# Kernel tuning notes

Hardware: AMD Instinct MI355X
Metric: run time of the kernel (lower is better)

Reference implementation:

```python
import jax, jax.numpy as jnp
import numpy as np
from jax import lax

B, TZ, TT = 16, 2048, 512
D, DFF, L, V, HEADS = 256, 1024, 6, 512, 4
CH, HID, K, FLOWS, G = 256, 256, 5, 4, 256
PAD_ID = 0
NEG = -1e9
SCALE = 0.02


def setup_inputs():
    key = jax.random.key(0)
    ks = jax.random.split(key, 20)
    n = lambda i, shape, s=SCALE: jax.random.normal(ks[i], shape, jnp.float32) * s
    return {
        'z': jax.random.normal(ks[0], (B, TZ, CH), jnp.float32),
        'text': jax.random.randint(ks[1], (B, TT), 1, V),  # low=1 so no pad tokens
        'cond': jax.random.normal(ks[2], (B, G), jnp.float32),
        'embed': n(3, (V, D), 1.0),
        'wq': n(4, (L, D, D)), 'wk': n(5, (L, D, D)), 'wv': n(6, (L, D, D)), 'wo': n(7, (L, D, D)),
        'bq': jnp.zeros((L, D)), 'bk': jnp.zeros((L, D)), 'bv': jnp.zeros((L, D)), 'bo': jnp.zeros((L, D)),
        'ln1_g': jnp.ones((L, D)), 'ln1_b': jnp.zeros((L, D)),
        'ln2_g': jnp.ones((L, D)), 'ln2_b': jnp.zeros((L, D)),
        'w1': n(8, (L, D, DFF)), 'b1': jnp.zeros((L, DFF)),
        'w2': n(9, (L, DFF, D)), 'b2': jnp.zeros((L, D)),
        'mu_w': n(10, (D, D)), 'mu_b': jnp.zeros((D,)),
        'lv_w': n(11, (D, D)), 'lv_b': jnp.zeros((D,)),
        'flow_in': n(12, (FLOWS, CH // 2, HID)), 'flow_in_b': jnp.zeros((FLOWS, HID)),
        'flow_cond': n(13, (FLOWS, G, HID)),
        'flow_conv': n(14, (FLOWS, K, HID, HID)), 'flow_conv_b': jnp.zeros((FLOWS, HID)),
        'flow_out': n(15, (FLOWS, HID, CH // 2)), 'flow_out_b': jnp.zeros((FLOWS, CH // 2)),
    }


def _pos_encoding(length, d):
    pos = np.arange(length)[:, None].astype(np.float32)
    i = np.arange(d)[None, :]
    angle = pos / np.power(10000.0, (2 * (i // 2)) / d)
    pe = np.where(i % 2 == 0, np.sin(angle), np.cos(angle))
    return jnp.asarray(pe, jnp.float32)


def _ln(x, g, b):
    m = jnp.mean(x, -1, keepdims=True)
    v = jnp.var(x, -1, keepdims=True)
    return g * (x - m) * lax.rsqrt(v + 1e-6) + b


def _mha(x, wq, wk, wv, wo, bq, bk, bv, bo, bias):
    Bq, T, _ = x.shape
    dh = D // HEADS
    heads = lambda y: y.reshape(Bq, T, HEADS, dh).transpose(0, 2, 1, 3)
    q, k, v = heads(x @ wq + bq), heads(x @ wk + bk), heads(x @ wv + bv)
    scores = jnp.einsum('bhqd,bhkd->bhqk', q, k) / jnp.sqrt(jnp.float32(dh)) + bias
    attn = jax.nn.softmax(scores, axis=-1)
    out = jnp.einsum('bhqk,bhkd->bhqd', attn, v).transpose(0, 2, 1, 3).reshape(Bq, T, D)
    return out @ wo + bo


def _mas_path(logp, text_mask):
    # Viterbi monotonic alignment: each latent frame t maps to text index j(t),
    # j nondecreasing with steps in {0, 1}, start at 0, end at last valid token.
    Bq, Tz, Tt = logp.shape
    Q0 = jnp.where(jnp.arange(Tt) == 0, logp[:, 0, :], NEG)

    def fwd(Q, lt):
        Qs = jnp.concatenate([jnp.full((Bq, 1), NEG, Q.dtype), Q[:, :-1]], axis=1)
        return lt + jnp.maximum(Q, Qs), Qs > Q  # choice True => came from j-1

    _, choices = lax.scan(fwd, Q0, jnp.swapaxes(logp, 0, 1)[1:])  # [Tz-1,B,Tt]
    j_last = jnp.sum(text_mask, axis=1).astype(jnp.int32) - 1

    def bwd(j, ch):
        c = jnp.take_along_axis(ch, j[:, None], axis=1)[:, 0]
        jp = j - c.astype(jnp.int32)
        return jp, jp

    _, path_rev = lax.scan(bwd, j_last, choices[::-1])
    path = jnp.concatenate([path_rev[::-1], j_last[None]], axis=0)  # [Tz,B]
    return jnp.swapaxes(path, 0, 1)


def _forward(z, text, cond, embed, wq, wk, wv, wo, bq, bk, bv, bo, ln1_g, ln1_b, ln2_g, ln2_b,
             w1, b1, w2, b2, mu_w, mu_b, lv_w, lv_b,
             flow_in, flow_in_b, flow_cond, flow_conv, flow_conv_b, flow_out, flow_out_b):
    text_mask = text != PAD_ID  # [B,TT]
    bias = jnp.where(text_mask[:, None, None, :], 0.0, NEG)
    # text encoder: scaled embedding + sinusoidal PE + post-LN transformer blocks
    h = embed[text] * jnp.sqrt(jnp.float32(D)) + _pos_encoding(TT, D)[None]
    for l in range(L):
        h = _ln(h + _mha(h, wq[l], wk[l], wv[l], wo[l], bq[l], bk[l], bv[l], bo[l], bias), ln1_g[l], ln1_b[l])
        ffn = jax.nn.relu(h @ w1[l] + b1[l]) @ w2[l] + b2[l]
        h = _ln(h + ffn, ln2_g[l], ln2_b[l])
    mu = h @ mu_w + mu_b
    logvar = h @ lv_w + lv_b
    # residual coupling flows (mean-only, conditioned on global vector)
    zc = z
    for f in range(FLOWS):
        x0, x1 = jnp.split(zc, 2, axis=-1)
        hh = x0 @ flow_in[f] + flow_in_b[f] + (cond @ flow_cond[f])[:, None, :]
        hh = jnp.tanh(lax.conv_general_dilated(hh, flow_conv[f], (1,), 'SAME', rhs_dilation=(1,),
                                               dimension_numbers=('NWC', 'WIO', 'NWC')) + flow_conv_b[f])
        m = hh @ flow_out[f] + flow_out_b[f]
        zc = jnp.concatenate([x1 + m, x0], axis=-1)  # coupling + flip
    # gaussian log-likelihood between latent frames and text distributions
    spr = jnp.exp(-logvar)  # [B,TT,D]
    nc1 = jnp.sum(-0.5 * jnp.log(2.0 * jnp.pi) - 0.5 * logvar, axis=-1)  # [B,TT]
    nc2 = jnp.einsum('btd,bjd->btj', -0.5 * zc * zc, spr)
    nc3 = jnp.einsum('btd,bjd->btj', zc, mu * spr)
    nc4 = jnp.sum(-0.5 * mu * mu * spr, axis=-1)  # [B,TT]
    logp = nc1[:, None, :] + nc2 + nc3 + nc4[:, None, :]  # [B,TZ,TT]
    logp = jnp.where(text_mask[:, None, :], logp, NEG)
    path = _mas_path(logp, text_mask)  # [B,TZ] int32
    ctx = mu[jnp.arange(B)[:, None], path]  # expand text mu along latent time
    return ctx, h


def reference(z, text, cond, embed, wq, wk, wv, wo, bq, bk, bv, bo, ln1_g, ln1_b, ln2_g, ln2_b,
              w1, b1, w2, b2, mu_w, mu_b, lv_w, lv_b,
              flow_in, flow_in_b, flow_cond, flow_conv, flow_conv_b, flow_out, flow_out_b):
    return _forward(z, text, cond, embed, wq, wk, wv, wo, bq, bk, bv, bo, ln1_g, ln1_b, ln2_g, ln2_b,
                    w1, b1, w2, b2, mu_w, mu_b, lv_w, lv_b,
                    flow_in, flow_in_b, flow_cond, flow_conv, flow_conv_b, flow_out, flow_out_b)
```

## Files before the change

### kernel.cpp

```cpp
#include <hip/hip_runtime.h>

#define BB 16
#define TZ_ 2048
#define TT_ 512
#define D_ 256
#define DFF_ 1024
#define L_ 6
#define HEADS_ 4
#define DH_ 64
#define CH_ 256
#define HID_ 256
#define KCV 5
#define FLOWS_ 4
#define G_ 256
#define NEGF (-1000000000.0f)
#define LOG2PI 1.8378770664093453f

typedef unsigned short u16;
typedef __attribute__((ext_vector_type(8))) short short8v;
typedef __attribute__((ext_vector_type(4))) float f32x4;

__device__ __forceinline__ float wsum(float v){
#pragma unroll
  for (int o = 32; o; o >>= 1) v += __shfl_xor(v, o);
  return v;
}
__device__ __forceinline__ u16 f2bf(float x){
  unsigned u = __float_as_uint(x);
  return (u16)((u + 0x7FFFu + ((u >> 16) & 1u)) >> 16);
}
__device__ __forceinline__ float bf2f(u16 h){
  return __uint_as_float(((unsigned)h) << 16);
}
__device__ __forceinline__ unsigned pk2f(float a, float b){
  return __builtin_amdgcn_perm(__float_as_uint(b), __float_as_uint(a), 0x07060302u);
}
__device__ __forceinline__ float trnc(float f){
  return __uint_as_float(__float_as_uint(f) & 0xFFFF0000u);
}
__device__ __forceinline__ void cvt8t(float4 x, float4 y, uint4 &hi, uint4 &lo){
  hi.x = pk2f(x.x, x.y); hi.y = pk2f(x.z, x.w);
  hi.z = pk2f(y.x, y.y); hi.w = pk2f(y.z, y.w);
  float r0 = x.x - trnc(x.x), r1 = x.y - trnc(x.y), r2 = x.z - trnc(x.z), r3 = x.w - trnc(x.w);
  float r4 = y.x - trnc(y.x), r5 = y.y - trnc(y.y), r6 = y.z - trnc(y.z), r7 = y.w - trnc(y.w);
  lo.x = pk2f(r0, r1); lo.y = pk2f(r2, r3); lo.z = pk2f(r4, r5); lo.w = pk2f(r6, r7);
}
__device__ __forceinline__ unsigned rneh(float f){
  unsigned v = __float_as_uint(f);
  return (v + 0x7FFFu + ((v >> 16) & 1u)) & 0xFFFF0000u;
}
__device__ __forceinline__ void cvt8r(float4 x, float4 y, uint4 &hi, uint4 &lo){
  unsigned h0=rneh(x.x), h1=rneh(x.y), h2=rneh(x.z), h3=rneh(x.w);
  unsigned h4=rneh(y.x), h5=rneh(y.y), h6=rneh(y.z), h7=rneh(y.w);
  hi.x = h1 | (h0>>16); hi.y = h3 | (h2>>16); hi.z = h5 | (h4>>16); hi.w = h7 | (h6>>16);
  float r0 = x.x - __uint_as_float(h0), r1 = x.y - __uint_as_float(h1);
  float r2 = x.z - __uint_as_float(h2), r3 = x.w - __uint_as_float(h3);
  float r4 = y.x - __uint_as_float(h4), r5 = y.y - __uint_as_float(h5);
  float r6 = y.z - __uint_as_float(h6), r7 = y.w - __uint_as_float(h7);
  lo.x = pk2f(r0, r1); lo.y = pk2f(r2, r3); lo.z = pk2f(r4, r5); lo.w = pk2f(r6, r7);
}

__global__ void k_pe(float* __restrict__ pe){
  int t = blockIdx.x, d = threadIdx.x;
  double e = (double)(2*(d>>1)) / (double)D_;
  double ang = (double)t * pow(10000.0, -e);
  pe[t*D_ + d] = (float)(((d&1)==0) ? sin(ang) : cos(ang));
}
__global__ void k_embed(const int* __restrict__ text, const float* __restrict__ emb,
                        const float* __restrict__ pe, float* __restrict__ h){
  int row = blockIdx.x, d = threadIdx.x;
  h[(size_t)row*D_ + d] = emb[(size_t)text[row]*D_ + d]*16.0f + pe[(row%TT_)*D_ + d];
}

__global__ __launch_bounds__(256) void k_wt(
  const float* __restrict__ wq, const float* __restrict__ wk,
  const float* __restrict__ wv, const float* __restrict__ wo,
  const float* __restrict__ mu_w, const float* __restrict__ lv_w,
  const float* __restrict__ w1, const float* __restrict__ w2,
  float* __restrict__ QKVT, float* __restrict__ OT, float* __restrict__ MULVT,
  float* __restrict__ W1T, float* __restrict__ W2T)
{
  __shared__ float td[64][65];
  const int s = blockIdx.y, tile = blockIdx.x, t = threadIdx.x;
  const float* inb; float* outb; int istride, ostride;
  if (s < 24){
    int l = s>>2, wsel = s&3;
    const float* w = (wsel==0?wq:wsel==1?wk:wsel==2?wv:wo);
    inb = w + (size_t)l*65536; istride = 256;
    if (wsel < 3) outb = QKVT + (size_t)l*196608 + wsel*65536;
    else          outb = OT   + (size_t)l*65536;
    ostride = 256;
  } else if (s < 26){
    inb = (s==24 ? mu_w : lv_w); istride = 256;
    outb = MULVT + (size_t)(s-24)*65536; ostride = 256;
  } else if (s < 50){
    int idx = s-26, l = idx>>2, b2 = idx&3;
    inb = w1 + (size_t)l*262144 + b2*256; istride = 1024;
    outb = W1T + (size_t)l*262144 + (size_t)b2*65536; ostride = 256;
  } else {
    int idx = s-50, l = idx>>2, b2 = idx&3;
    inb = w2 + (size_t)l*262144 + (size_t)b2*65536; istride = 256;
    outb = W2T + (size_t)l*262144 + b2*256; ostride = 1024;
  }
  const int kt = (tile>>2)*64, nt = (tile&3)*64;
  const int r = t>>2, cq = (t&3)*16;
#pragma unroll
  for (int c=0;c<16;c+=4){
    float4 v = *(const float4*)(inb + (size_t)(kt + r)*istride + nt + cq + c);
    td[r][cq+c+0]=v.x; td[r][cq+c+1]=v.y; td[r][cq+c+2]=v.z; td[r][cq+c+3]=v.w;
  }
  __syncthreads();
#pragma unroll
  for (int c=0;c<16;c+=4){
    float4 v = make_float4(td[cq+c+0][r], td[cq+c+1][r], td[cq+c+2][r], td[cq+c+3][r]);
    *(float4*)(outb + (size_t)(nt + r)*ostride + kt + cq + c) = v;
  }
}

__global__ __launch_bounds__(256) void k_vt(const float* __restrict__ QKV, float* __restrict__ VT){
  __shared__ float td[64][65];
  const int b = blockIdx.z, dt = blockIdx.x, jt = blockIdx.y, t = threadIdx.x;
  const float* inb = QKV + (size_t)b*512*768 + 512;
  float* outb = VT + (size_t)b*131072;
  const int r = t>>2, cq = (t&3)*16;
#pragma unroll
  for (int c=0;c<16;c+=4){
    float4 v = *(const float4*)(inb + (size_t)(jt*64 + r)*768 + dt*64 + cq + c);
    td[r][cq+c+0]=v.x; td[r][cq+c+1]=v.y; td[r][cq+c+2]=v.z; td[r][cq+c+3]=v.w;
  }
  __syncthreads();
#pragma unroll
  for (int c=0;c<16;c+=4){
    float4 v = make_float4(td[cq+c+0][r], td[cq+c+1][r], td[cq+c+2][r], td[cq+c+3][r]);
    *(float4*)(outb + (size_t)(dt*64 + r)*512 + jt*64 + cq + c) = v;
  }
}

__global__ void k_bcat(const float* __restrict__ bq, const float* __restrict__ bk,
                       const float* __restrict__ bv, const float* __restrict__ mu_b,
                       const float* __restrict__ lv_b,
                       float* __restrict__ BQKV, float* __restrict__ MULVB){
  int i = blockIdx.x*256 + threadIdx.x;
  if (i < 4608){
    int l = i/768, c = i%768;
    float v = c<256 ? bq[l*256+c] : (c<512 ? bk[l*256+c-256] : bv[l*256+c-512]);
    BQKV[i] = v;
  } else if (i < 5120){
    int c = i-4608;
    MULVB[c] = c<256 ? mu_b[c] : lv_b[c-256];
  }
}

template<int WN, int EPI, int AM, int BMD>
__global__ __launch_bounds__(256,2) void k_mg(
  const void* __restrict__ Ap, const void* __restrict__ ApL, int lda, int azhi, int azlo,
  const void* __restrict__ Bp, const void* __restrict__ BpL, int ldb, int bzhi, int bzlo,
  const float* __restrict__ bias, const int* __restrict__ text,
  const float* __restrict__ nc1v, const float* __restrict__ nc4v,
  float* __restrict__ C, int ldc, int czhi, int czlo, int K)
{
  constexpr int BN = WN*32;
  __shared__ u16 AH[4096], AL[4096];
  __shared__ u16 BH[BN*32], BL[BN*32];
  char* AHB=(char*)AH; char* ALB=(char*)AL; char* BHB=(char*)BH; char* BLB=(char*)BL;
  const int t = threadIdx.x, z = blockIdx.z;
  const int m0 = blockIdx.y*128, n0 = blockIdx.x*BN;
  const size_t aoff = (size_t)(z>>2)*azhi + (size_t)(z&3)*azlo;
  const size_t boff = (size_t)(z>>2)*bzhi + (size_t)(z&3)*bzlo;
  const size_t coff = (size_t)(z>>2)*czhi + (size_t)(z&3)*czlo;
  const int w = t>>6, l = t&63;
  const int wr = (w>>1)*64, wc = (w&1)*(WN*16);
  const int lr = l&15, lg = l>>4;
  const int srow = t>>1, sseg = t&1;
  const int q  = (srow>>1)&3;
  const int wo0 = srow*64 + ((((sseg<<1)|0)^q)<<4);
  const int wo1 = srow*64 + ((((sseg<<1)|1)^q)<<4);
  const bool bact = (WN==4) || (t < 128);
  const int qa = ((wr+lr)>>1)&3, qb2 = ((wc+lr)>>1)&3;
  const int raBase = (wr+lr)*64 + ((lg^qa)<<4);
  const int rbBase = (wc+lr)*64 + ((lg^qb2)<<4);

  const float* Af = nullptr; const u16* AfH = nullptr; const u16* AfL = nullptr;
  if constexpr (AM==0 || AM==2){ Af = (const float*)Ap + aoff; }
  else { AfH = (const u16*)Ap + aoff; AfL = (const u16*)ApL + aoff; }
  const float* Bf = nullptr; const u16* BfH = nullptr; const u16* BfL = nullptr;
  if constexpr (BMD==0){ Bf = (const float*)Bp + boff; }
  else { BfH = (const u16*)Bp + boff; BfL = (const u16*)BpL + boff; }

  float4 sa0, sa1, sa2, sa3;
  uint4  pah0, pah1, pal0, pal1;
  float4 sb0, sb1, sb2, sb3;
  uint4  pbh0, pbh1, pbl0, pbl1;

  auto LOADA = [&](int kk){
    if constexpr (AM==0){
      const float* p = Af + (size_t)(m0+srow)*lda + kk + sseg*16;
      sa0=*(const float4*)p; sa1=*(const float4*)(p+4);
      sa2=*(const float4*)(p+8); sa3=*(const float4*)(p+12);
    } else if constexpr (AM==1){
      const u16* ph = AfH + (size_t)(m0+srow)*lda + kk + sseg*16;
      const u16* pl = AfL + (size_t)(m0+srow)*lda + kk + sseg*16;
      pah0 = *(const uint4*)ph; pah1 = *(const uint4*)(ph+8);
      pal0 = *(const uint4*)pl; pal1 = *(const uint4*)(pl+8);
    } else {
      int kg = kk + sseg*16;
      const float* p = Af + (size_t)(m0+srow)*lda + (kg < 256 ? kg : kg - 256);
      sa0=*(const float4*)p; sa1=*(const float4*)(p+4);
      sa2=*(const float4*)(p+8); sa3=*(const float4*)(p+12);
    }
  };
  auto LOADB = [&](int kk){
    if constexpr (BMD==0){
      const float* p = Bf + (size_t)(n0+srow)*ldb + kk + sseg*16;
      sb0=*(const float4*)p; sb1=*(const float4*)(p+4);
      sb2=*(const float4*)(p+8); sb3=*(const float4*)(p+12);
    } else {
      const u16* ph = BfH + (size_t)(n0+srow)*ldb + kk + sseg*16;
      const u16* pl = BfL + (size_t)(n0+srow)*ldb + kk + sseg*16;
      pbh0 = *(const uint4*)ph; pbh1 = *(const uint4*)(ph+8);
      pbl0 = *(const uint4*)pl; pbl1 = *(const uint4*)(pl+8);
    }
  };
  auto WRITEA = [&](int kk){
    uint4 ahi0, ahi1, alo0, alo1;
    if constexpr (AM==0){
      cvt8t(sa0,sa1,ahi0,alo0); cvt8t(sa2,sa3,ahi1,alo1);
    } else if constexpr (AM==1){
      ahi0=pah0; ahi1=pah1; alo0=pal0; alo1=pal1;
    } else {
      float4 a0=sa0, a1=sa1, a2=sa2, a3=sa3;
      int kg = kk + sseg*16;
      if (kg >= 256){
        a0.x=-0.5f*a0.x*a0.x; a0.y=-0.5f*a0.y*a0.y; a0.z=-0.5f*a0.z*a0.z; a0.w=-0.5f*a0.w*a0.w;
        a1.x=-0.5f*a1.x*a1.x; a1.y=-0.5f*a1.y*a1.y; a1.z=-0.5f*a1.z*a1.z; a1.w=-0.5f*a1.w*a1.w;
        a2.x=-0.5f*a2.x*a2.x; a2.y=-0.5f*a2.y*a2.y; a2.z=-0.5f*a2.z*a2.z; a2.w=-0.5f*a2.w*a2.w;
        a3.x=-0.5f*a3.x*a3.x; a3.y=-0.5f*a3.y*a3.y; a3.z=-0.5f*a3.z*a3.z; a3.w=-0.5f*a3.w*a3.w;
      }
      cvt8r(a0,a1,ahi0,alo0); cvt8r(a2,a3,ahi1,alo1);
    }
    *(uint4*)(AHB + wo0) = ahi0;  *(uint4*)(AHB + wo1) = ahi1;
    *(uint4*)(ALB + wo0) = alo0;  *(uint4*)(ALB + wo1) = alo1;
  };
  auto WRITEB = [&](){
    uint4 bhi0, bhi1, blo0, blo1;
    if constexpr (BMD==0){
      cvt8t(sb0,sb1,bhi0,blo0); cvt8t(sb2,sb3,bhi1,blo1);
    } else {
      bhi0=pbh0; bhi1=pbh1; blo0=pbl0; blo1=pbl1;
    }
    *(uint4*)(BHB + wo0) = bhi0;  *(uint4*)(BHB + wo1) = bhi1;
    *(uint4*)(BLB + wo0) = blo0;  *(uint4*)(BLB + wo1) = blo1;
  };

  f32x4 acc[4][WN];
#pragma unroll
  for (int i=0;i<4;i++)
#pragma unroll
    for (int j=0;j<WN;j++) acc[i][j] = (f32x4){0.f,0.f,0.f,0.f};

  LOADA(0);
  if (bact) LOADB(0);
  for (int k0 = 0; k0 < K; k0 += 32){
    __syncthreads();
    WRITEA(k0);
    if (bact) WRITEB();
    if (k0 + 32 < K){ LOADA(k0+32); if (bact) LOADB(k0+32); }
    __syncthreads();
    short8v fah[4], fal[4], fbh[WN], fbl[WN];
#pragma unroll
    for (int i=0;i<4;i++){
      fah[i] = *(short8v*)(AHB + raBase + i*1024);
      fal[i] = *(short8v*)(ALB + raBase + i*1024);
    }
#pragma unroll
    for (int j=0;j<WN;j++){
      fbh[j] = *(short8v*)(BHB + rbBase + j*1024);
      fbl[j] = *(short8v*)(BLB + rbBase + j*1024);
    }
#pragma unroll
    for (int i=0;i<4;i++)
#pragma unroll
      for (int j=0;j<WN;j++){
        acc[i][j] = __builtin_amdgcn_mfma_f32_16x16x32_bf16(fah[i], fbh[j], acc[i][j], 0,0,0);
        acc[i][j] = __builtin_amdgcn_mfma_f32_16x16x32_bf16(fal[i], fbh[j], acc[i][j], 0,0,0);
        acc[i][j] = __builtin_amdgcn_mfma_f32_16x16x32_bf16(fah[i], fbl[j], acc[i][j], 0,0,0);
      }
  }

#pragma unroll
  for (int i=0;i<4;i++){
    int mm0 = m0 + wr + i*16 + (lg<<2);
#pragma unroll
    for (int j=0;j<WN;j++){
      int nn = n0 + wc + j*16 + lr;
      float bs = 0.f; float ncb = 0.f; bool msk = true;
      if (EPI==0 || EPI==1) bs = bias ? bias[nn] : 0.f;
      if (EPI==2) msk = (text[(z>>2)*TT_ + nn] != 0);
      if (EPI==3){ ncb = nc1v[z*TT_+nn] + nc4v[z*TT_+nn]; msk = (text[z*TT_+nn] != 0); }
      f32x4 v = acc[i][j];
#pragma unroll
      for (int r=0;r<4;r++){
        int m = mm0 + r;
        float x;
        if (EPI==0)      x = v[r] + bs;
        else if (EPI==1) x = fmaxf(v[r] + bs, 0.f);
        else if (EPI==2) x = v[r]*0.125f + (msk ? 0.f : NEGF);
        else             x = msk ? (v[r] + ncb) : NEGF;
        C[coff + (size_t)m*ldc + nn] = x;
      }
    }
  }
}

__global__ __launch_bounds__(256) void k_softmax(float* __restrict__ S){
  size_t row = (size_t)blockIdx.x*4 + (threadIdx.x >> 6);
  float* p = S + row*TT_;
  int ln = threadIdx.x & 63;
  float4 a = *(float4*)(p + ln*8);
  float4 b = *(float4*)(p + ln*8 + 4);
  float x[8] = {a.x,a.y,a.z,a.w,b.x,b.y,b.z,b.w};
  float m = x[0];
#pragma unroll
  for (int i=1;i<8;i++) m = fmaxf(m, x[i]);
#pragma unroll
  for (int o2=32;o2;o2>>=1) m = fmaxf(m, __shfl_xor(m, o2));
  float s = 0.f;
#pragma unroll
  for (int i=0;i<8;i++){ x[i] = expf(x[i]-m); s += x[i]; }
  s = wsum(s);
  float inv = 1.0f/s;
  *(float4*)(p + ln*8)     = make_float4(x[0]*inv, x[1]*inv, x[2]*inv, x[3]*inv);
  *(float4*)(p + ln*8 + 4) = make_float4(x[4]*inv, x[5]*inv, x[6]*inv, x[7]*inv);
}

__global__ __launch_bounds__(256) void k_lnres(const float* __restrict__ y,
  const float* __restrict__ g, const float* __restrict__ bb, float* __restrict__ h){
  size_t row = blockIdx.x; int d = threadIdx.x;
  float v = h[row*D_ + d] + y[row*D_ + d];
  float s = wsum(v), s2 = wsum(v*v);
  __shared__ float r1[4], r2[4];
  int w = d >> 6;
  if ((d & 63) == 0){ r1[w] = s; r2[w] = s2; }
  __syncthreads();
  s  = r1[0]+r1[1]+r1[2]+r1[3];
  s2 = r2[0]+r2[1]+r2[2]+r2[3];
  float mean = s * (1.0f/D_);
  float var  = s2 * (1.0f/D_) - mean*mean;
  float inv  = rsqrtf(var + 1e-6f);
  h[row*D_ + d] = g[d]*(v - mean)*inv + bb[d];
}

__global__ __launch_bounds__(256) void k_prep(const float* __restrict__ mulv,
  u16* __restrict__ b2h, u16* __restrict__ b2l,
  float* __restrict__ nc1, float* __restrict__ nc4){
  size_t row = blockIdx.x; int d = threadIdx.x;
  float m = mulv[row*512 + d];
  float lv = mulv[row*512 + 256 + d];
  float sp = expf(-lv);
  float ms = m*sp;
  float s1 = wsum(lv), s2 = wsum(m*ms);
  __shared__ float r1[4], r2[4];
  int w = d >> 6;
  if ((d&63)==0){ r1[w]=s1; r2[w]=s2; }
  __syncthreads();
  if (d == 0){
    nc1[row] = -0.5f*((float)D_*LOG2PI + (r1[0]+r1[1]+r1[2]+r1[3]));
    nc4[row] = -0.5f*(r2[0]+r2[1]+r2[2]+r2[3]);
  }
  unsigned hm = rneh(ms);
  b2h[row*512 + d] = (u16)(hm>>16);
  b2l[row*512 + d] = f2bf(ms - __uint_as_float(hm));
  unsigned hs = rneh(sp);
  b2h[row*512 + 256 + d] = (u16)(hs>>16);
  b2l[row*512 + 256 + d] = f2bf(sp - __uint_as_float(hs));
}

__global__ __launch_bounds__(256) void k_fprep(
  const float* __restrict__ win, const float* __restrict__ wconv, const float* __restrict__ wout,
  u16* __restrict__ WITH, u16* __restrict__ WITL,
  u16* __restrict__ WCTH, u16* __restrict__ WCTL,
  u16* __restrict__ WOTH, u16* __restrict__ WOTL,
  const float* __restrict__ zsrc, u16* __restrict__ xh, u16* __restrict__ xl,
  const float* __restrict__ cond, const float* __restrict__ fcw, float* __restrict__ condp)
{
  const int bid = blockIdx.x, t = threadIdx.x;
  if (bid < 1536){
    int i = bid*256 + t;
    float wv2; u16 *dh, *dl; int idx;
    if (i < 32768){
      int n = i >> 7, k = i & 127;
      wv2 = win[k*256 + n]; dh = WITH; dl = WITL; idx = i;
    } else if (i < 360448){
      int jj = i - 32768;
      int o = jj / 1280, r = jj - o*1280;
      wv2 = wconv[(size_t)r*256 + o]; dh = WCTH; dl = WCTL; idx = jj;
    } else {
      int jj = i - 360448;
      int o = jj >> 8, k = jj & 255;
      wv2 = wout[k*128 + o]; dh = WOTH; dl = WOTL; idx = jj;
    }
    u16 hh = f2bf(wv2);
    dh[idx] = hh;
    dl[idx] = f2bf(wv2 - bf2f(hh));
  } else if (bid < 3584){
    size_t i = ((size_t)(bid-1536)*256 + t) << 3;
    size_t m2 = i >> 7; int k = (int)(i & 127);
    const float* src = zsrc + m2*256 + k;
    float4 a = *(const float4*)src; float4 b2 = *(const float4*)(src+4);
    float vv[8] = {a.x,a.y,a.z,a.w,b2.x,b2.y,b2.z,b2.w};
    short8v oh, ol;
#pragma unroll
    for (int r=0;r<8;r++){
      u16 hh = f2bf(vv[r]);
      oh[r] = (short)hh;
      ol[r] = (short)f2bf(vv[r] - bf2f(hh));
    }
    *(short8v*)(xh + i) = oh;
    *(short8v*)(xl + i) = ol;
  } else {
    int b = bid - 3584, n = t;
    float s = 0.f;
    for (int k2=0;k2<G_;k2++) s = fmaf(cond[b*G_ + k2], fcw[k2*HID_ + n], s);
    condp[b*HID_ + n] = s;
  }
}

__global__ void k_padzero2(u16* __restrict__ XpH, u16* __restrict__ XpL){
  int i = blockIdx.x*256 + threadIdx.x;
  u16* P = (i >> 14) ? XpL : XpH;
  int ii = i & 16383;
  int b = ii >> 10, rr = (ii >> 8) & 3, c = ii & 255;
  int row = (rr < 2) ? rr : (2048 + rr);
  P[((size_t)b*2052 + row)*256 + c] = 0;
}

template<int EPI, int SPLITOUT>
__global__ __launch_bounds__(256,2) void k_mf2(
  const u16* __restrict__ Ah, const u16* __restrict__ Al, int lda, int padA,
  const u16* __restrict__ Bh, const u16* __restrict__ Bl, int ldb,
  const float* __restrict__ bias, const float* __restrict__ cnd,
  void* __restrict__ CH, void* __restrict__ CL, int ldc, int padC, int K)
{
  __shared__ u16 AsmH[4096], AsmL[4096], BsmH[4096], BsmL[4096];
  char* AHB=(char*)AsmH; char* ALB=(char*)AsmL;
  char* BHB=(char*)BsmH; char* BLB=(char*)BsmL;
  const int t = threadIdx.x;
  const int m0 = blockIdx.y << 7, n0 = blockIdx.x << 7;
  const int w = t >> 6, l = t & 63;
  const int wr = (w >> 1) << 6, wc = (w & 1) << 6;
  const int lr = l & 15, lg = l >> 4;
  const int srow = t >> 1, sseg = t & 1;
  const int q = (srow >> 1) & 3;
  const int wo0 = srow*64 + ((((sseg<<1)|0) ^ q) << 4);
  const int wo1 = srow*64 + ((((sseg<<1)|1) ^ q) << 4);
  const int am = m0 + srow;
  const size_t aoff = (size_t)(am + padA*(am >> 11))*lda + (sseg << 4);
  const u16* AhP = Ah + aoff;
  const u16* AlP = Al + aoff;
  const size_t boff = (size_t)(n0 + srow)*ldb + (sseg << 4);
  const u16* BhP = Bh + boff;
  const u16* BlP = Bl + boff;
  const int qa = ((wr + lr) >> 1) & 3, qb = ((wc + lr) >> 1) & 3;
  const int raBase = (wr + lr)*64 + ((lg ^ qa) << 4);
  const int rbBase = (wc + lr)*64 + ((lg ^ qb) << 4);
  f32x4 acc[4][4];
#pragma unroll
  for (int i=0;i<4;i++)
#pragma unroll
    for (int j=0;j<4;j++) acc[i][j] = (f32x4){0.f,0.f,0.f,0.f};

  float4 sah0, sah1, sal0, sal1, sbh0, sbh1, sbl0, sbl1;
  auto LOADF = [&](int kk){
    sah0 = *(const float4*)(AhP + kk); sah1 = *(const float4*)(AhP + kk + 8);
    sal0 = *(const float4*)(AlP + kk); sal1 = *(const float4*)(AlP + kk + 8);
    sbh0 = *(const float4*)(BhP + kk); sbh1 = *(const float4*)(BhP + kk + 8);
    sbl0 = *(const float4*)(BlP + kk); sbl1 = *(const float4*)(BlP + kk + 8);
  };

  LOADF(0);
  for (int k0 = 0; k0 < K; k0 += 32){
    __syncthreads();
    *(float4*)(AHB + wo0) = sah0;  *(float4*)(AHB + wo1) = sah1;
    *(float4*)(ALB + wo0) = sal0;  *(float4*)(ALB + wo1) = sal1;
    *(float4*)(BHB + wo0) = sbh0;  *(float4*)(BHB + wo1) = sbh1;
    *(float4*)(BLB + wo0) = sbl0;  *(float4*)(BLB + wo1) = sbl1;
    if (k0 + 32 < K) LOADF(k0 + 32);
    __syncthreads();
    short8v fah[4], fal[4], fbh[4], fbl[4];
#pragma unroll
    for (int i=0;i<4;i++){
      fah[i] = *(short8v*)(AHB + raBase + i*1024);
      fal[i] = *(short8v*)(ALB + raBase + i*1024);
    }
#pragma unroll
    for (int j=0;j<4;j++){
      fbh[j] = *(short8v*)(BHB + rbBase + j*1024);
      fbl[j] = *(short8v*)(BLB + rbBase + j*1024);
    }
#pragma unroll
    for (int i=0;i<4;i++)
#pragma unroll
      for (int j=0;j<4;j++){
        acc[i][j] = __builtin_amdgcn_mfma_f32_16x16x32_bf16(fah[i], fbh[j], acc[i][j], 0, 0, 0);
        acc[i][j] = __builtin_amdgcn_mfma_f32_16x16x32_bf16(fal[i], fbh[j], acc[i][j], 0, 0, 0);
        acc[i][j] = __builtin_amdgcn_mfma_f32_16x16x32_bf16(fah[i], fbl[j], acc[i][j], 0, 0, 0);
      }
  }

#pragma unroll
  for (int i=0;i<4;i++){
    int mbase = m0 + wr + i*16 + (lg << 2);
#pragma unroll
    for (int j=0;j<4;j++){
      int nn = n0 + wc + j*16 + lr;
      float bs = bias[nn];
      f32x4 v = acc[i][j];
#pragma unroll
      for (int r=0;r<4;r++){
        int m = mbase + r;
        float x = v[r] + bs;
        if (EPI == 1) x += cnd[((m >> 11) << 8) + nn];
        if (EPI == 2) x = tanhf(x);
        if (EPI == 3) x += cnd[(size_t)m*256 + 128 + nn];
        size_t ro = (size_t)(m + padC*(m >> 11))*ldc + nn;
        if (SPLITOUT){
          u16 xh = f2bf(x);
          ((u16*)CH)[ro] = xh;
          ((u16*)CL)[ro] = f2bf(x - bf2f(xh));
        } else {
          ((float*)CH)[ro] = x;
          if (EPI == 3)
            ((float*)CH)[(size_t)m*ldc + 128 + nn] = cnd[(size_t)m*256 + nn];
        }
      }
    }
  }
}

#define MCH 8
#define NCHK (TZ_/MCH)

__device__ __forceinline__ void mas_row(float4 u0, float4 u1, float* Q, int ln, int tr,
                                        unsigned char* __restrict__ cb){
  if (tr == 0){
    if (ln == 0) Q[0] = u0.x;
    return;
  }
  float v[8] = {u0.x,u0.y,u0.z,u0.w,u1.x,u1.y,u1.z,u1.w};
  float qp = __shfl_up(Q[7], 1);
  if (ln == 0) qp = NEGF;
  unsigned bits = 0; float qs = qp;
#pragma unroll
  for (int i=0;i<8;i++){
    float old = Q[i];
    if (qs > old) bits |= (1u<<i);
    Q[i] = v[i] + fmaxf(old, qs);
    qs = old;
  }
  cb[(size_t)(tr-1)*64 + ln] = (unsigned char)bits;
}

__global__ __launch_bounds__(512) void k_mas(const float* __restrict__ lp,
  const int* __restrict__ text, unsigned char* __restrict__ cho, int* __restrict__ path)
{
  const int b = blockIdx.x, t = threadIdx.x, ln = t & 63;
  const float* L = lp + (size_t)b*TZ_*TT_;
  __shared__ float buf[3*MCH*TT_];
  __shared__ __align__(16) unsigned char lch[3*4096];
  const int frow = t >> 6, lc = t & 63;
  const size_t gsrc = (size_t)frow*TT_ + lc*8;
  char* base = (char*)&buf[0];
  const int wrB = frow*2048 + lc*16;
  unsigned char* cb = cho + (size_t)b*TZ_*64;

  {
    float4 a0 = *(const float4*)(L + gsrc);
    float4 a1 = *(const float4*)(L + gsrc + 4);
    float4 c0 = *(const float4*)(L + (size_t)MCH*TT_ + gsrc);
    float4 c1 = *(const float4*)(L + (size_t)MCH*TT_ + gsrc + 4);
    *(float4*)(base + 0*16384 + wrB)        = a0;
    *(float4*)(base + 0*16384 + wrB + 1024) = a1;
    *(float4*)(base + 1*16384 + wrB)        = c0;
    *(float4*)(base + 1*16384 + wrB + 1024) = c1;
  }
  float4 pA0 = *(const float4*)(L + (size_t)2*MCH*TT_ + gsrc);
  float4 pA1 = *(const float4*)(L + (size_t)2*MCH*TT_ + gsrc + 4);
  float4 pB0 = *(const float4*)(L + (size_t)3*MCH*TT_ + gsrc);
  float4 pB1 = *(const float4*)(L + (size_t)3*MCH*TT_ + gsrc + 4);
  __syncthreads();

  float Q[8];
#pragma unroll
  for (int i=0;i<8;i++) Q[i] = NEGF;
  const int rB = ln*16;
  float4 hA0,hA1,hA2,hA3,hA4,hA5,hA6,hA7;
  float4 hB0,hB1,hB2,hB3,hB4,hB5,hB6,hB7;
  if (t < 64){
    hA0 = *(float4*)(base + 0*2048 + rB); hA1 = *(float4*)(base + 0*2048 + rB + 1024);
    hA2 = *(float4*)(base + 1*2048 + rB); hA3 = *(float4*)(base + 1*2048 + rB + 1024);
    hA4 = *(float4*)(base + 2*2048 + rB); hA5 = *(float4*)(base + 2*2048 + rB + 1024);
    hA6 = *(float4*)(base + 3*2048 + rB); hA7 = *(float4*)(base + 3*2048 + rB + 1024);
  }
  int cur = 0;
  for (int ch = 0; ch < NCHK; ch++){
    int wIdx = cur + 2; if (wIdx >= 3) wIdx -= 3;
    if (ch + 2 < NCHK){
      char* wb = base + wIdx*16384;
      if (ch & 1){ *(float4*)(wb + wrB) = pB0; *(float4*)(wb + wrB + 1024) = pB1; }
      else       { *(float4*)(wb + wrB) = pA0; *(float4*)(wb + wrB + 1024) = pA1; }
    }
    if (ch + 4 < NCHK){
      const float* src = L + (size_t)(ch+4)*MCH*TT_ + gsrc;
      if (ch & 1){ pB0 = *(const float4*)src; pB1 = *(const float4*)(src+4); }
      else       { pA0 = *(const float4*)src; pA1 = *(const float4*)(src+4); }
    }
    if (t < 64){
      char* cbuf = base + cur*16384;
      int nIdx = cur + 1; if (nIdx >= 3) nIdx -= 3;
      char* nbuf = base + nIdx*16384;
      hB0 = *(float4*)(cbuf + 4*2048 + rB); hB1 = *(float4*)(cbuf + 4*2048 + rB + 1024);
      hB2 = *(float4*)(cbuf + 5*2048 + rB); hB3 = *(float4*)(cbuf + 5*2048 + rB + 1024);
      hB4 = *(float4*)(cbuf + 6*2048 + rB); hB5 = *(float4*)(cbuf + 6*2048 + rB + 1024);
      hB6 = *(float4*)(cbuf + 7*2048 + rB); hB7 = *(float4*)(cbuf + 7*2048 + rB + 1024);
      mas_row(hA0,hA1,Q,ln, ch*MCH+0, cb);
      mas_row(hA2,hA3,Q,ln, ch*MCH+1, cb);
      mas_row(hA4,hA5,Q,ln, ch*MCH+2, cb);
      mas_row(hA6,hA7,Q,ln, ch*MCH+3, cb);
      hA0 = *(float4*)(nbuf + 0*2048 + rB); hA1 = *(float4*)(nbuf + 0*2048 + rB + 1024);
      hA2 = *(float4*)(nbuf + 1*2048 + rB); hA3 = *(float4*)(nbuf + 1*2048 + rB + 1024);
      hA4 = *(float4*)(nbuf + 2*2048 + rB); hA5 = *(float4*)(nbuf + 2*2048 + rB + 1024);
      hA6 = *(float4*)(nbuf + 3*2048 + rB); hA7 = *(float4*)(nbuf + 3*2048 + rB + 1024);
      mas_row(hB0,hB1,Q,ln, ch*MCH+4, cb);
      mas_row(hB2,hB3,Q,ln, ch*MCH+5, cb);
      mas_row(hB4,hB5,Q,ln, ch*MCH+6, cb);
      mas_row(hB6,hB7,Q,ln, ch*MCH+7, cb);
    }
    __syncthreads();
    cur++; if (cur >= 3) cur = 0;
  }

  int jl = 0;
  if (t < 64){
    int cnt = 0;
#pragma unroll
    for (int i=0;i<8;i++) cnt += (text[b*TT_ + ln*8 + i] != 0) ? 1 : 0;
#pragma unroll
    for (int o2=32;o2;o2>>=1) cnt += __shfl_xor(cnt, o2);
    jl = cnt - 1;
  }
  if (t == 0) path[b*TZ_ + TZ_-1] = jl;
  __syncthreads();

  const int NP = TZ_ - 1;
  const int NH = 32;
  uint* lchU = (uint*)lch;
  const uint* cbU = (const uint*)cb;
  {
#pragma unroll
    for (int k = 0; k < 2; k++){
      int d = t + k*512;
      int p = d >> 4;
      lchU[d]        = cbU[(size_t)(2046 - p)*16 + (d & 15)];
      lchU[1024 + d] = cbU[(size_t)(2046 - (64 + p))*16 + (d & 15)];
    }
  }
  uint uA0, uA1, uB0, uB1;
  {
    int d0 = t, d1 = t + 512;
    uA0 = cbU[(size_t)(2046 - (128 + (d0>>4)))*16 + (d0 & 15)];
    uA1 = cbU[(size_t)(2046 - (128 + (d1>>4)))*16 + (d1 & 15)];
    uB0 = cbU[(size_t)(2046 - (192 + (d0>>4)))*16 + (d0 & 15)];
    uB1 = cbU[(size_t)(2046 - (192 + (d1>>4)))*16 + (d1 & 15)];
  }
  __syncthreads();

  int j = jl;
  unsigned rb0[8], rb1[8]; int rc[8];
  if (t == 0){
#pragma unroll
    for (int qd=0; qd<8; qd++){
      int cHi = jl >> 3;
      int cLo = (cHi > 0) ? cHi - 1 : 0;
      rb1[qd] = lch[qd*64 + cHi];
      rb0[qd] = lch[qd*64 + cLo];
      rc[qd]  = cHi;
    }
  }
  for (int H = 0; H < NH; H++){
    if (H + 2 < NH){
      int wslot = (H + 2) % 3;
      uint* wb = lchU + wslot*1024;
      if (H & 1){ wb[t] = uB0; wb[t+512] = uB1; }
      else      { wb[t] = uA0; wb[t+512] = uA1; }
    }
    if (H + 4 < NH){
      int d0 = t, d1 = t + 512;
      int bse = (H+4)*64;
      int p0 = bse + (d0>>4), p1 = bse + (d1>>4);
      uint v0 = (p0 <= 2046) ? cbU[(size_t)(2046 - p0)*16 + (d0 & 15)] : 0u;
      uint v1 = (p1 <= 2046) ? cbU[(size_t)(2046 - p1)*16 + (d1 & 15)] : 0u;
      if (H & 1){ uB0 = v0; uB1 = v1; }
      else      { uA0 = v0; uA1 = v1; }
    }
    if (t == 0){
      int pbase = H*64;
#pragma unroll 8
      for (int s = 0; s < 64; s++){
        int p = pbase + s;
        if (p < NP){
          int r = s & 7;
          int jb = j >> 3;
          unsigned byte = (jb == rc[r]) ? rb1[r] : rb0[r];
          j -= (int)((byte >> (j & 7)) & 1u);
          path[b*TZ_ + 2046 - p] = j;
          int pn = p + 8;
          if (pn < NP){
            int hn = (pn >> 6) % 3, sn = pn & 63;
            int cHi = j >> 3;
            int cLo = (cHi > 0) ? cHi - 1 : 0;
            rb1[r] = lch[hn*4096 + sn*64 + cHi];
            rb0[r] = lch[hn*4096 + sn*64 + cLo];
            rc[r]  = cHi;
          }
        }
      }
    }
    __syncthreads();
  }
}

__global__ void k_gather(const float* __restrict__ mulv, const int* __restrict__ path,
  const float* __restrict__ h, float* __restrict__ out){
  size_t i = (size_t)blockIdx.x*256 + threadIdx.x;
  const size_t N4 = (size_t)BB*TZ_*(D_/4);
  const size_t H4 = (size_t)BB*TT_*(D_/4);
  if (i < N4){
    size_t row = i >> 6; int c = (int)(i & 63);
    int b = (int)(row >> 11);
    int pj = path[row];
    ((float4*)out)[i] = *(const float4*)(mulv + ((size_t)b*TT_ + pj)*512 + (size_t)c*4);
  } else if (i < N4 + H4){
    size_t k2 = i - N4;
    ((float4*)out)[i] = ((const float4*)h)[k2];
  }
}

extern "C" void kernel_launch(void* const* d_in, const int* in_sizes, int n_in,
                              void* d_out, int out_size, void* d_ws, size_t ws_size,
                              hipStream_t stream)
{
  (void)in_sizes; (void)n_in; (void)out_size; (void)ws_size;
  const float* z      = (const float*)d_in[0];
  const int*   text   = (const int*)  d_in[1];
  const float* cond   = (const float*)d_in[2];
  const float* emb    = (const float*)d_in[3];
  const float* wq     = (const float*)d_in[4];
  const float* wk     = (const float*)d_in[5];
  const float* wv     = (const float*)d_in[6];
  const float* wo     = (const float*)d_in[7];
  const float* bq     = (const float*)d_in[8];
  const float* bk     = (const float*)d_in[9];
  const float* bv     = (const float*)d_in[10];
  const float* bo     = (const float*)d_in[11];
  const float* ln1g   = (const float*)d_in[12];
  const float* ln1b   = (const float*)d_in[13];
  const float* ln2g   = (const float*)d_in[14];
  const float* ln2b   = (const float*)d_in[15];
  const float* w1     = (const float*)d_in[16];
  const float* b1     = (const float*)d_in[17];
  const float* w2     = (const float*)d_in[18];
  const float* b2     = (const float*)d_in[19];
  const float* mu_w   = (const float*)d_in[20];
  const float* mu_b   = (const float*)d_in[21];
  const float* lv_w   = (const float*)d_in[22];
  const float* lv_b   = (const float*)d_in[23];
  const float* f_in   = (const float*)d_in[24];
  const float* f_in_b = (const float*)d_in[25];
  const float* f_cond = (const float*)d_in[26];
  const float* f_conv = (const float*)d_in[27];
  const float* f_convb= (const float*)d_in[28];
  const float* f_out  = (const float*)d_in[29];
  const float* f_outb = (const float*)d_in[30];

  float* ws = (float*)d_ws;
  size_t o = 0;
  float* PE   = ws + o; o += (size_t)131072;
  float* H    = ws + o; o += (size_t)2097152;
  float* MULV = ws + o; o += (size_t)4194304;
  float* NC1  = ws + o; o += (size_t)8192;
  float* NC4  = ws + o; o += (size_t)8192;
  float* CONDP= ws + o; o += (size_t)4096;
  int*   PATH = (int*)(ws + o); o += (size_t)32768;
  u16*  B2H  = (u16*)(ws + o); o += (size_t)2097152;
  u16*  B2L  = (u16*)(ws + o); o += (size_t)2097152;
  float* BIGS = ws + o; o += (size_t)16777216;
  float* BUF1 = ws + o; o += (size_t)4587520;
  float* BUF2 = ws + o; o += (size_t)10485760;
  float* ZCA  = ws + o; o += (size_t)8388608;
  float* ZCB  = ws + o; o += (size_t)8388608;

  float* QKV = BUF2;
  float* Yb  = QKV + 6291456;
  float* VT  = Yb + 2097152;
  float* ATTO= QKV;
  float* QKVT = ZCA;
  float* OT   = QKVT + 1179648;
  float* W1T  = OT + 393216;
  float* W2T  = W1T + 1572864;
  float* MULVT= W2T + 1572864;
  float* BQKV = MULVT + 131072;
  float* MULVB= BQKV + 4608;
  u16*  X0H = (u16*)BUF1;
  u16*  X0L = X0H + 4194304;
  u16*  WITH = X0L + 4194304;
  u16*  WITL = WITH + 32768;
  u16*  WCTH = WITL + 32768;
  u16*  WCTL = WCTH + 327680;
  u16*  WOTH = WCTL + 327680;
  u16*  WOTL = WOTH + 32768;
  u16*  XpH = (u16*)BIGS;
  u16*  XpL = XpH + 8404992;
  u16*  H2H = (u16*)BUF2;
  u16*  H2L = H2H + 8388608;
  unsigned char* CHO = (unsigned char*)ZCA;

  k_pe   <<<dim3(TT_),    dim3(D_), 0, stream>>>(PE);
  k_embed<<<dim3(BB*TT_), dim3(D_), 0, stream>>>(text, emb, PE, H);
  k_wt   <<<dim3(16,74), 256, 0, stream>>>(wq,wk,wv,wo,mu_w,lv_w,w1,w2, QKVT,OT,MULVT,W1T,W2T);
  k_bcat <<<dim3(20), 256, 0, stream>>>(bq,bk,bv,mu_b,lv_b, BQKV, MULVB);

  for (int l=0;l<L_;l++){
    k_mg<4,0,0,0><<<dim3(6,64,1),256,0,stream>>>(
      H, nullptr, 256, 0,0,  QKVT + (size_t)l*196608, nullptr, 256, 0,0,
      BQKV + l*768, nullptr, nullptr, nullptr, QKV, 768, 0,0, 256);
    k_vt <<<dim3(4,8,16),256,0,stream>>>(QKV, VT);
    k_mg<4,2,0,0><<<dim3(4,4,64),256,0,stream>>>(
      QKV, nullptr, 768, 393216, 64,  QKV+256, nullptr, 768, 393216, 64,
      nullptr, text, nullptr, nullptr, BIGS, 512, 1048576, 262144, 64);
    k_softmax<<<dim3(BB*HEADS_*TT_/4),256,0,stream>>>(BIGS);
    k_mg<2,0,0,0><<<dim3(1,4,64),256,0,stream>>>(
      BIGS, nullptr, 512, 1048576, 262144,  VT, nullptr, 512, 131072, 32768,
      nullptr, nullptr, nullptr, nullptr, Yb, 256, 131072, 64, 512);
    k_mg<4,0,0,0><<<dim3(2,64,1),256,0,stream>>>(
      Yb, nullptr, 256, 0,0,  OT + (size_t)l*65536, nullptr, 256, 0,0,
      bo + l*256, nullptr, nullptr, nullptr, ATTO, 256, 0,0, 256);
    k_lnres<<<dim3(BB*TT_),256,0,stream>>>(ATTO, ln1g+l*D_, ln1b+l*D_, H);
    k_mg<4,1,0,0><<<dim3(8,64,1),256,0,stream>>>(
      H, nullptr, 256, 0,0,  W1T + (size_t)l*262144, nullptr, 256, 0,0,
      b1 + l*1024, nullptr, nullptr, nullptr, BIGS, 1024, 0,0, 256);
    k_mg<4,0,0,0><<<dim3(2,64,1),256,0,stream>>>(
      BIGS, nullptr, 1024, 0,0,  W2T + (size_t)l*262144, nullptr, 1024, 0,0,
      b2 + l*256, nullptr, nullptr, nullptr, ATTO, 256, 0,0, 1024);
    k_lnres<<<dim3(BB*TT_),256,0,stream>>>(ATTO, ln2g+l*D_, ln2b+l*D_, H);
  }

  k_mg<4,0,0,0><<<dim3(4,64,1),256,0,stream>>>(
    H, nullptr, 256, 0,0,  MULVT, nullptr, 256, 0,0,
    MULVB, nullptr, nullptr, nullptr, MULV, 512, 0,0, 256);
  k_prep<<<dim3(BB*TT_),256,0,stream>>>(MULV, B2H, B2L, NC1, NC4);

  k_padzero2<<<dim3(128),256,0,stream>>>(XpH, XpL);
  const float* zsrc = z;
  for (int f=0; f<FLOWS_; f++){
    k_fprep<<<dim3(3600),256,0,stream>>>(
        f_in + (size_t)f*(CH_/2)*HID_, f_conv + (size_t)f*KCV*HID_*HID_,
        f_out + (size_t)f*HID_*(CH_/2),
        WITH, WITL, WCTH, WCTL, WOTH, WOTL,
        zsrc, X0H, X0L,
        cond, f_cond + (size_t)f*G_*HID_, CONDP);
    k_mf2<1,1><<<dim3(2,256),256,0,stream>>>(X0H, X0L, 128, 0, WITH, WITL, 128,
        f_in_b + f*HID_, CONDP, (void*)(XpH + 512), (void*)(XpL + 512), 256, 4, 128);
    k_mf2<2,1><<<dim3(2,256),256,0,stream>>>(XpH, XpL, 256, 4, WCTH, WCTL, 1280,
        f_convb + f*HID_, nullptr, (void*)H2H, (void*)H2L, 256, 0, 1280);
    float* zdst = (f & 1) ? ZCB : ZCA;
    k_mf2<3,0><<<dim3(1,256),256,0,stream>>>(H2H, H2L, 256, 0, WOTH, WOTL, 256,
        f_outb + f*(CH_/2), zsrc, (void*)zdst, nullptr, 256, 0, 256);
    zsrc = zdst;
  }

  k_mg<4,3,2,1><<<dim3(4,16,16),256,0,stream>>>(
    zsrc, nullptr, 256, 2097152, 524288,
    B2H, B2L, 512, 1048576, 262144,
    nullptr, text, NC1, NC4, BIGS, 512, 4194304, 1048576, 512);

  k_mas<<<dim3(BB),512,0,stream>>>(BIGS, text, CHO, PATH);
  k_gather<<<dim3((BB*TZ_*D_/4 + BB*TT_*D_/4)/256),256,0,stream>>>(MULV, PATH, H, (float*)d_out);
}
```

Baseline: 2.320 ms.

## Run MAS kernel as a single wavefront with register prefetch, dropping LDS staging

```diff
diff --git a/kernel.cpp b/kernel.cpp
--- a/kernel.cpp
+++ b/kernel.cpp
@@ -537,15 +537,8 @@
   }
 }
 
-#define MCH 8
-#define NCHK (TZ_/MCH)
-
-__device__ __forceinline__ void mas_row(float4 u0, float4 u1, float* Q, int ln, int tr,
-                                        unsigned char* __restrict__ cb){
-  if (tr == 0){
-    if (ln == 0) Q[0] = u0.x;
-    return;
-  }
+__device__ __forceinline__ void mas_row1(float4 u0, float4 u1, float* Q, int ln, int tr,
+                                         unsigned char* __restrict__ cb){
   float v[8] = {u0.x,u0.y,u0.z,u0.w,u1.x,u1.y,u1.z,u1.w};
   float qp = __shfl_up(Q[7], 1);
   if (ln == 0) qp = NEGF;
@@ -560,123 +553,96 @@
   cb[(size_t)(tr-1)*64 + ln] = (unsigned char)bits;
 }
 
-__global__ __launch_bounds__(512) void k_mas(const float* __restrict__ lp,
+__global__ __launch_bounds__(64,1) void k_mas(const float* __restrict__ lp,
   const int* __restrict__ text, unsigned char* __restrict__ cho, int* __restrict__ path)
 {
-  const int b = blockIdx.x, t = threadIdx.x, ln = t & 63;
+  const int b = blockIdx.x, ln = threadIdx.x;
   const float* L = lp + (size_t)b*TZ_*TT_;
-  __shared__ float buf[3*MCH*TT_];
+  const float* Lr = L + ln*8;
+  unsigned char* cb = cho + (size_t)b*TZ_*64;
   __shared__ __align__(16) unsigned char lch[3*4096];
-  const int frow = t >> 6, lc = t & 63;
-  const size_t gsrc = (size_t)frow*TT_ + lc*8;
-  char* base = (char*)&buf[0];
-  const int wrB = frow*2048 + lc*16;
-  unsigned char* cb = cho + (size_t)b*TZ_*64;
-
-  {
-    float4 a0 = *(const float4*)(L + gsrc);
-    float4 a1 = *(const float4*)(L + gsrc + 4);
-    float4 c0 = *(const float4*)(L + (size_t)MCH*TT_ + gsrc);
-    float4 c1 = *(const float4*)(L + (size_t)MCH*TT_ + gsrc + 4);
-    *(float4*)(base + 0*16384 + wrB)        = a0;
-    *(float4*)(base + 0*16384 + wrB + 1024) = a1;
-    *(float4*)(base + 1*16384 + wrB)        = c0;
-    *(float4*)(base + 1*16384 + wrB + 1024) = c1;
-  }
-  float4 pA0 = *(const float4*)(L + (size_t)2*MCH*TT_ + gsrc);
-  float4 pA1 = *(const float4*)(L + (size_t)2*MCH*TT_ + gsrc + 4);
-  float4 pB0 = *(const float4*)(L + (size_t)3*MCH*TT_ + gsrc);
-  float4 pB1 = *(const float4*)(L + (size_t)3*MCH*TT_ + gsrc + 4);
+
+  float Q[8];
+#pragma unroll
+  for (int i=0;i<8;i++) Q[i] = NEGF;
+  if (ln == 0) Q[0] = L[0];
+
+  float4 P0a = *(const float4*)(Lr + (size_t)1*TT_), P0b = *(const float4*)(Lr + (size_t)1*TT_ + 4);
+  float4 P1a = *(const float4*)(Lr + (size_t)2*TT_), P1b = *(const float4*)(Lr + (size_t)2*TT_ + 4);
+  float4 P2a = *(const float4*)(Lr + (size_t)3*TT_), P2b = *(const float4*)(Lr + (size_t)3*TT_ + 4);
+  float4 P3a = *(const float4*)(Lr + (size_t)4*TT_), P3b = *(const float4*)(Lr + (size_t)4*TT_ + 4);
+  float4 P4a = *(const float4*)(Lr + (size_t)5*TT_), P4b = *(const float4*)(Lr + (size_t)5*TT_ + 4);
+  float4 P5a = *(const float4*)(Lr + (size_t)6*TT_), P5b = *(const float4*)(Lr + (size_t)6*TT_ + 4);
+  float4 P6a = *(const float4*)(Lr + (size_t)7*TT_), P6b = *(const float4*)(Lr + (size_t)7*TT_ + 4);
+  float4 P7a = *(const float4*)(Lr + (size_t)8*TT_), P7b = *(const float4*)(Lr + (size_t)8*TT_ + 4);
+
+  int t0 = 1;
+#define MAS_SLOT(Pa, Pb, OFF) \
+    mas_row1(Pa, Pb, Q, ln, t0 + OFF, cb); \
+    { const float* _s = Lr + (size_t)(t0 + OFF + 8)*TT_; \
+      Pa = *(const float4*)_s; Pb = *(const float4*)(_s + 4); } \
+    __builtin_amdgcn_sched_barrier(0);
+  for (; t0 + 15 <= TZ_ - 1; t0 += 8){
+    MAS_SLOT(P0a, P0b, 0)
+    MAS_SLOT(P1a, P1b, 1)
+    MAS_SLOT(P2a, P2b, 2)
+    MAS_SLOT(P3a, P3b, 3)
+    MAS_SLOT(P4a, P4b, 4)
+    MAS_SLOT(P5a, P5b, 5)
+    MAS_SLOT(P6a, P6b, 6)
+    MAS_SLOT(P7a, P7b, 7)
+  }
+#undef MAS_SLOT
+  mas_row1(P0a,P0b,Q,ln,t0+0,cb);
+  mas_row1(P1a,P1b,Q,ln,t0+1,cb);
+  mas_row1(P2a,P2b,Q,ln,t0+2,cb);
+  mas_row1(P3a,P3b,Q,ln,t0+3,cb);
+  mas_row1(P4a,P4b,Q,ln,t0+4,cb);
+  mas_row1(P5a,P5b,Q,ln,t0+5,cb);
+  mas_row1(P6a,P6b,Q,ln,t0+6,cb);
+  mas_row1(P7a,P7b,Q,ln,t0+7,cb);
+  for (int t = t0 + 8; t < TZ_; t++){
+    const float* s = Lr + (size_t)t*TT_;
+    float4 a = *(const float4*)s;
+    float4 c = *(const float4*)(s + 4);
+    mas_row1(a, c, Q, ln, t, cb);
+  }
+
+  int cnt = 0;
+#pragma unroll
+  for (int i=0;i<8;i++) cnt += (text[b*TT_ + ln*8 + i] != 0) ? 1 : 0;
+#pragma unroll
+  for (int o2=32;o2;o2>>=1) cnt += __shfl_xor(cnt, o2);
+  const int jl = cnt - 1;
+  if (ln == 0) path[b*TZ_ + TZ_-1] = jl;
+
   __syncthreads();
 
-  float Q[8];
-#pragma unroll
-  for (int i=0;i<8;i++) Q[i] = NEGF;
-  const int rB = ln*16;
-  float4 hA0,hA1,hA2,hA3,hA4,hA5,hA6,hA7;
-  float4 hB0,hB1,hB2,hB3,hB4,hB5,hB6,hB7;
-  if (t < 64){
-    hA0 = *(float4*)(base + 0*2048 + rB); hA1 = *(float4*)(base + 0*2048 + rB + 1024);
-    hA2 = *(float4*)(base + 1*2048 + rB); hA3 = *(float4*)(base + 1*2048 + rB + 1024);
-    hA4 = *(float4*)(base + 2*2048 + rB); hA5 = *(float4*)(base + 2*2048 + rB + 1024);
-    hA6 = *(float4*)(base + 3*2048 + rB); hA7 = *(float4*)(base + 3*2048 + rB + 1024);
-  }
-  int cur = 0;
-  for (int ch = 0; ch < NCHK; ch++){
-    int wIdx = cur + 2; if (wIdx >= 3) wIdx -= 3;
-    if (ch + 2 < NCHK){
-      char* wb = base + wIdx*16384;
-      if (ch & 1){ *(float4*)(wb + wrB) = pB0; *(float4*)(wb + wrB + 1024) = pB1; }
-      else       { *(float4*)(wb + wrB) = pA0; *(float4*)(wb + wrB + 1024) = pA1; }
-    }
-    if (ch + 4 < NCHK){
-      const float* src = L + (size_t)(ch+4)*MCH*TT_ + gsrc;
-      if (ch & 1){ pB0 = *(const float4*)src; pB1 = *(const float4*)(src+4); }
-      else       { pA0 = *(const float4*)src; pA1 = *(const float4*)(src+4); }
-    }
-    if (t < 64){
-      char* cbuf = base + cur*16384;
-      int nIdx = cur + 1; if (nIdx >= 3) nIdx -= 3;
-      char* nbuf = base + nIdx*16384;
-      hB0 = *(float4*)(cbuf + 4*2048 + rB); hB1 = *(float4*)(cbuf + 4*2048 + rB + 1024);
-      hB2 = *(float4*)(cbuf + 5*2048 + rB); hB3 = *(float4*)(cbuf + 5*2048 + rB + 1024);
-      hB4 = *(float4*)(cbuf + 6*2048 + rB); hB5 = *(float4*)(cbuf + 6*2048 + rB + 1024);
-      hB6 = *(float4*)(cbuf + 7*2048 + rB); hB7 = *(float4*)(cbuf + 7*2048 + rB + 1024);
-      mas_row(hA0,hA1,Q,ln, ch*MCH+0, cb);
-      mas_row(hA2,hA3,Q,ln, ch*MCH+1, cb);
-      mas_row(hA4,hA5,Q,ln, ch*MCH+2, cb);
-      mas_row(hA6,hA7,Q,ln, ch*MCH+3, cb);
-      hA0 = *(float4*)(nbuf + 0*2048 + rB); hA1 = *(float4*)(nbuf + 0*2048 + rB + 1024);
-      hA2 = *(float4*)(nbuf + 1*2048 + rB); hA3 = *(float4*)(nbuf + 1*2048 + rB + 1024);
-      hA4 = *(float4*)(nbuf + 2*2048 + rB); hA5 = *(float4*)(nbuf + 2*2048 + rB + 1024);
-      hA6 = *(float4*)(nbuf + 3*2048 + rB); hA7 = *(float4*)(nbuf + 3*2048 + rB + 1024);
-      mas_row(hB0,hB1,Q,ln, ch*MCH+4, cb);
-      mas_row(hB2,hB3,Q,ln, ch*MCH+5, cb);
-      mas_row(hB4,hB5,Q,ln, ch*MCH+6, cb);
-      mas_row(hB6,hB7,Q,ln, ch*MCH+7, cb);
-    }
-    __syncthreads();
-    cur++; if (cur >= 3) cur = 0;
-  }
-
-  int jl = 0;
-  if (t < 64){
-    int cnt = 0;
-#pragma unroll
-    for (int i=0;i<8;i++) cnt += (text[b*TT_ + ln*8 + i] != 0) ? 1 : 0;
-#pragma unroll
-    for (int o2=32;o2;o2>>=1) cnt += __shfl_xor(cnt, o2);
-    jl = cnt - 1;
-  }
-  if (t == 0) path[b*TZ_ + TZ_-1] = jl;
-  __syncthreads();
-
   const int NP = TZ_ - 1;
-  const int NH = 32;
   uint* lchU = (uint*)lch;
   const uint* cbU = (const uint*)cb;
   {
-#pragma unroll
-    for (int k = 0; k < 2; k++){
-      int d = t + k*512;
-      int p = d >> 4;
-      lchU[d]        = cbU[(size_t)(2046 - p)*16 + (d & 15)];
-      lchU[1024 + d] = cbU[(size_t)(2046 - (64 + p))*16 + (d & 15)];
-    }
-  }
-  uint uA0, uA1, uB0, uB1;
+    int r0 = 2046 - ln;
+#pragma unroll
+    for (int k=0;k<4;k++)
+      *(uint4*)&lchU[0*1024 + ln*16 + k*4] = *(const uint4*)&cbU[(size_t)r0*16 + k*4];
+    int r1 = 2046 - (64 + ln);
+#pragma unroll
+    for (int k=0;k<4;k++)
+      *(uint4*)&lchU[1*1024 + ln*16 + k*4] = *(const uint4*)&cbU[(size_t)r1*16 + k*4];
+  }
+  uint4 su0, su1, su2, su3;
   {
-    int d0 = t, d1 = t + 512;
-    uA0 = cbU[(size_t)(2046 - (128 + (d0>>4)))*16 + (d0 & 15)];
-    uA1 = cbU[(size_t)(2046 - (128 + (d1>>4)))*16 + (d1 & 15)];
-    uB0 = cbU[(size_t)(2046 - (192 + (d0>>4)))*16 + (d0 & 15)];
-    uB1 = cbU[(size_t)(2046 - (192 + (d1>>4)))*16 + (d1 & 15)];
-  }
-  __syncthreads();
+    int r2 = 2046 - (128 + ln);
+    su0 = *(const uint4*)&cbU[(size_t)r2*16 + 0];
+    su1 = *(const uint4*)&cbU[(size_t)r2*16 + 4];
+    su2 = *(const uint4*)&cbU[(size_t)r2*16 + 8];
+    su3 = *(const uint4*)&cbU[(size_t)r2*16 + 12];
+  }
 
   int j = jl;
   unsigned rb0[8], rb1[8]; int rc[8];
-  if (t == 0){
+  if (ln == 0){
 #pragma unroll
     for (int qd=0; qd<8; qd++){
       int cHi = jl >> 3;
@@ -686,23 +652,25 @@
       rc[qd]  = cHi;
     }
   }
-  for (int H = 0; H < NH; H++){
-    if (H + 2 < NH){
-      int wslot = (H + 2) % 3;
-      uint* wb = lchU + wslot*1024;
-      if (H & 1){ wb[t] = uB0; wb[t+512] = uB1; }
-      else      { wb[t] = uA0; wb[t+512] = uA1; }
-    }
-    if (H + 4 < NH){
-      int d0 = t, d1 = t + 512;
-      int bse = (H+4)*64;
-      int p0 = bse + (d0>>4), p1 = bse + (d1>>4);
-      uint v0 = (p0 <= 2046) ? cbU[(size_t)(2046 - p0)*16 + (d0 & 15)] : 0u;
-      uint v1 = (p1 <= 2046) ? cbU[(size_t)(2046 - p1)*16 + (d1 & 15)] : 0u;
-      if (H & 1){ uB0 = v0; uB1 = v1; }
-      else      { uA0 = v0; uA1 = v1; }
-    }
-    if (t == 0){
+  for (int H = 0; H < 32; H++){
+    if (H + 2 < 32){
+      uint* wb = lchU + ((H+2)%3)*1024;
+      *(uint4*)&wb[ln*16 + 0]  = su0;
+      *(uint4*)&wb[ln*16 + 4]  = su1;
+      *(uint4*)&wb[ln*16 + 8]  = su2;
+      *(uint4*)&wb[ln*16 + 12] = su3;
+    }
+    if (H + 3 < 32){
+      int p = (H+3)*64 + ln;
+      if (p <= 2046){
+        int r = 2046 - p;
+        su0 = *(const uint4*)&cbU[(size_t)r*16 + 0];
+        su1 = *(const uint4*)&cbU[(size_t)r*16 + 4];
+        su2 = *(const uint4*)&cbU[(size_t)r*16 + 8];
+        su3 = *(const uint4*)&cbU[(size_t)r*16 + 12];
+      }
+    }
+    if (ln == 0){
       int pbase = H*64;
 #pragma unroll 8
       for (int s = 0; s < 64; s++){
@@ -725,7 +693,6 @@
         }
       }
     }
-    __syncthreads();
   }
 }
 
@@ -883,6 +850,6 @@
     B2H, B2L, 512, 1048576, 262144,
     nullptr, text, NC1, NC4, BIGS, 512, 4194304, 1048576, 512);
 
-  k_mas<<<dim3(BB),512,0,stream>>>(BIGS, text, CHO, PATH);
+  k_mas<<<dim3(BB),64,0,stream>>>(BIGS, text, CHO, PATH);
   k_gather<<<dim3((BB*TZ_*D_/4 + BB*TT_*D_/4)/256),256,0,stream>>>(MULV, PATH, H, (float*)d_out);
 }
```

After: 2.249 ms. 1.03x faster.
